# Optimization experiments

Hardware: AMD Instinct MI355X
Metric: run time of the kernel (lower is better)

The kernel has to match this reference:

```python
import jax, jax.numpy as jnp
import numpy as np

S, B, D, H, F = 2048, 2, 1024, 16, 4096
HD = D // H
EPS = 1e-5


def setup_inputs() -> dict:
    key = jax.random.key(0)
    ks = jax.random.split(key, 16)
    sc_d = 1.0 / np.sqrt(D)
    sc_f = 1.0 / np.sqrt(F)
    return {
        "src": jax.random.normal(ks[0], (S, B, D), jnp.float32),
        # attention projections: Linear weights stored as [in, out] (y = x @ W + b)
        "Wq": jax.random.normal(ks[1], (D, D), jnp.float32) * sc_d,
        "bq": jnp.zeros((D,), jnp.float32),
        "Wk": jax.random.normal(ks[2], (D, D), jnp.float32) * sc_d,
        "bk": jnp.zeros((D,), jnp.float32),
        "Wv": jax.random.normal(ks[3], (D, D), jnp.float32) * sc_d,
        "bv": jnp.zeros((D,), jnp.float32),
        "Wo": jax.random.normal(ks[4], (D, D), jnp.float32) * sc_d,
        "bo": jnp.zeros((D,), jnp.float32),
        # norm1
        "g1": jnp.ones((D,), jnp.float32),
        "be1": jnp.zeros((D,), jnp.float32),
        # FFN
        "W1": jax.random.normal(ks[5], (D, F), jnp.float32) * sc_d,
        "bf1": jnp.zeros((F,), jnp.float32),
        "W2": jax.random.normal(ks[6], (F, D), jnp.float32) * sc_f,
        "bf2": jnp.zeros((D,), jnp.float32),
        # norm2
        "g2": jnp.ones((D,), jnp.float32),
        "be2": jnp.zeros((D,), jnp.float32),
    }


def _layernorm(x, g, b):
    m = jnp.mean(x, axis=-1, keepdims=True)
    v = jnp.mean(jnp.square(x - m), axis=-1, keepdims=True)
    return (x - m) * jax.lax.rsqrt(v + EPS) * g + b


def reference(src, Wq, bq, Wk, bk, Wv, bv, Wo, bo, g1, be1, W1, bf1, W2, bf2, g2, be2):
    # --- self attention (dropout_p=0 / eval mode => dropouts are identity) ---
    scaling = float(HD) ** -0.5
    q = (src @ Wq + bq) * scaling            # [S,B,D]
    k = src @ Wk + bk
    v = src @ Wv + bv
    # split heads: torch view(S, B*H, hd) == reshape(S, B, H, hd)
    qh = q.reshape(S, B, H, HD)
    kh = k.reshape(S, B, H, HD)
    vh = v.reshape(S, B, H, HD)
    scores = jnp.einsum("sbhd,tbhd->bhst", qh, kh)      # [B,H,S,S]
    attn = jax.nn.softmax(scores, axis=-1)
    ctx = jnp.einsum("bhst,tbhd->sbhd", attn, vh).reshape(S, B, D)
    attn_out = ctx @ Wo + bo
    # residual + norm1
    x = _layernorm(src + attn_out, g1, be1)
    # FFN (ReLU)
    ff = jax.nn.relu(x @ W1 + bf1) @ W2 + bf2
    # residual + norm2
    return _layernorm(x + ff, g2, be2)
```

## Files before the change

### kernel.cpp

```cpp
#include <hip/hip_runtime.h>
#include <hip/hip_bf16.h>

#define S_  2048
#define B_  2
#define D_  1024
#define H_  16
#define F_  4096
#define HD_ 64
#define NT_ (S_*B_)

typedef __attribute__((ext_vector_type(8))) short short8;
typedef __attribute__((ext_vector_type(4))) short short4v;
typedef __attribute__((ext_vector_type(4))) float f32x4;

#define MFMA16x16x32(a,b,c) __builtin_amdgcn_mfma_f32_16x16x32_bf16((a),(b),(c),0,0,0)

#define AS1C(p) ((const __attribute__((address_space(1))) void*)(p))
#define AS3(p)  ((__attribute__((address_space(3))) void*)(p))

__device__ __forceinline__ short f2b(float f) {
  union { float f; unsigned u; } x; x.f = f;
  unsigned r = x.u + 0x7FFFu + ((x.u >> 16) & 1u);
  return (short)(r >> 16);
}
__device__ __forceinline__ float b2f(short u) {
  union { unsigned u; float f; } x; x.u = ((unsigned)(unsigned short)u) << 16;
  return x.f;
}
__device__ __forceinline__ unsigned cvtpk(float a, float b) {
  unsigned r;
  asm("v_cvt_pk_bf16_f32 %0, %1, %2" : "=v"(r) : "v"(a), "v"(b));
  return r;
}
__device__ __forceinline__ float exp2fast(float x) {
  float r;
  asm("v_exp_f32 %0, %1" : "=v"(r) : "v"(x));
  return r;
}

__global__ __launch_bounds__(256) void to_bf16_k(const float* __restrict__ in,
                                                 short* __restrict__ out) {
  int i = (blockIdx.x * 256 + threadIdx.x) * 8;
  float4 a = *(const float4*)(in + i);
  float4 b = *(const float4*)(in + i + 4);
  short8 o;
  o[0] = f2b(a.x); o[1] = f2b(a.y); o[2] = f2b(a.z); o[3] = f2b(a.w);
  o[4] = f2b(b.x); o[5] = f2b(b.y); o[6] = f2b(b.z); o[7] = f2b(b.w);
  *(short8*)(out + i) = o;
}

__global__ __launch_bounds__(256) void transpose_to_bf16(const float* __restrict__ W,
                                                         short* __restrict__ Wt,
                                                         int K, int N, int colbase, int outK) {
  __shared__ short t[32][33];
  int tx = threadIdx.x & 31, ty = threadIdx.x >> 5;
  int kbase = blockIdx.y * 32, nbase = blockIdx.x * 32;
#pragma unroll
  for (int yy = 0; yy < 4; ++yy) {
    int kk = ty + yy * 8;
    t[kk][tx] = f2b(W[(size_t)(kbase + kk) * N + nbase + tx]);
  }
  __syncthreads();
#pragma unroll
  for (int yy = 0; yy < 4; ++yy) {
    int nn = ty + yy * 8;
    Wt[(size_t)(nbase + nn + colbase) * outK + kbase + tx] = t[tx][nn];
  }
}

template<int MODE>
__global__ __launch_bounds__(256, 2) void gemm_bt(
    const short* __restrict__ A, const short* __restrict__ Bt,
    int M, int N, int K, int lda,
    const float* __restrict__ bias0, const float* __restrict__ bias1,
    const float* __restrict__ bias2,
    float* __restrict__ outf,
    short* __restrict__ outq, short* __restrict__ outk, short* __restrict__ outv) {
  __shared__ __align__(16) short As[128 * 64];
  __shared__ __align__(16) short Bs[128 * 64];
  int tid = threadIdx.x;
  int lane = tid & 63, w = tid >> 6;
  int g = lane >> 4, r = lane & 15;
  int wm = w >> 1, wn = w & 1;

  int gx = gridDim.x, gy = gridDim.y;
  int nwg = gx * gy * gridDim.z;
  int flat = (blockIdx.z * gy + blockIdx.y) * gx + blockIdx.x;
  int cpx = nwg >> 3;
  int swz = (flat & 7) * cpx + (flat >> 3);
  int z = swz / (gx * gy);
  int rem = swz - z * gx * gy;
  int row0 = (rem / gx) * 128;
  int col0 = (rem % gx) * 128;
  size_t koff = (size_t)z * K;

  f32x4 acc[4][4];
#pragma unroll
  for (int m = 0; m < 4; ++m)
#pragma unroll
    for (int n = 0; n < 4; ++n) acc[m][n] = (f32x4){0.f, 0.f, 0.f, 0.f};

  for (int kt = 0; kt < K; kt += 64) {
#pragma unroll
    for (int p = 0; p < 4; ++p) {
      int idx = tid + p * 256;
      int row = idx >> 3, c = idx & 7;
      int scol = ((c ^ (row & 7)) << 3);
      __builtin_amdgcn_global_load_lds(AS1C(A  + (size_t)(row0 + row) * lda + koff + kt + scol),
                                       AS3(As + idx * 8), 16, 0, 0);
      __builtin_amdgcn_global_load_lds(AS1C(Bt + (size_t)(col0 + row) * lda + koff + kt + scol),
                                       AS3(Bs + idx * 8), 16, 0, 0);
    }
    __syncthreads();
    short8 af[4][2], bfr[4][2];
#pragma unroll
    for (int m = 0; m < 4; ++m)
#pragma unroll
      for (int kk = 0; kk < 2; ++kk) {
        int row = wm * 64 + m * 16 + r;
        af[m][kk] = *(const short8*)(As + row * 64 + (((kk * 4 + g) ^ (r & 7)) << 3));
      }
#pragma unroll
    for (int n = 0; n < 4; ++n)
#pragma unroll
      for (int kk = 0; kk < 2; ++kk) {
        int row = wn * 64 + n * 16 + r;
        bfr[n][kk] = *(const short8*)(Bs + row * 64 + (((kk * 4 + g) ^ (r & 7)) << 3));
      }
#pragma unroll
    for (int m = 0; m < 4; ++m)
#pragma unroll
      for (int n = 0; n < 4; ++n)
#pragma unroll
        for (int kk = 0; kk < 2; ++kk)
          acc[m][n] = MFMA16x16x32(af[m][kk], bfr[n][kk], acc[m][n]);
    __syncthreads();
  }

  int rb = row0 + wm * 64, cb = col0 + wn * 64;
#pragma unroll
  for (int m = 0; m < 4; ++m) {
#pragma unroll
    for (int n = 0; n < 4; ++n) {
#pragma unroll
      for (int j = 0; j < 4; ++j) {
        int row = rb + m * 16 + g * 4 + j;
        int col = cb + n * 16 + r;
        float v = acc[m][n][j];
        if (MODE == 0) {
          int s = row >> 1, b = row & 1;
          if (col < 1024) {
            float q = (v + bias0[col]) * (0.125f * 1.44269504088896f);
            int h = col >> 6, hd = col & 63;
            outq[((size_t)(b * H_ + h) * S_ + s) * HD_ + hd] = f2b(q);
          } else if (col < 2048) {
            int c2 = col - 1024;
            float kk = v + bias1[c2];
            int h = c2 >> 6, hd = c2 & 63;
            outk[((size_t)(b * H_ + h) * S_ + s) * HD_ + hd] = f2b(kk);
          } else {
            int c2 = col - 2048;
            float vv = v + bias2[c2];
            int h = c2 >> 6, hd = c2 & 63;
            outv[((size_t)(b * H_ + h) * HD_ + hd) * S_ + s] = f2b(vv);
          }
        } else if (MODE == 2) {
          size_t o = (size_t)row * N + col;
          float t = v + bias0[col];
          outq[o] = f2b(t > 0.f ? t : 0.f);
        } else {
          outf[(size_t)z * M * N + (size_t)row * N + col] = v;
        }
      }
    }
  }
}

__global__ __launch_bounds__(256, 4) void flash_attn(const short* __restrict__ Q,
                                                     const short* __restrict__ Kb,
                                                     const short* __restrict__ Vt,
                                                     short* __restrict__ ctx) {
  __shared__ __align__(16) short Ks[2][64 * 64];
  __shared__ __align__(16) short Vs[2][64 * 64];
  __shared__ __align__(16) short P[4][16][64];
  int tid = threadIdx.x;
  int lane = tid & 63, w = tid >> 6;
  int g = lane >> 4, r = lane & 15;
  int f = blockIdx.x;
  int xcd = f & 7, loc = f >> 3;
  int bh = xcd * 4 + (loc >> 5);
  int qt = loc & 31;
  const short* qp = Q  + (size_t)bh * S_ * HD_;
  const short* kp = Kb + (size_t)bh * S_ * HD_;
  const short* vp = Vt + (size_t)bh * HD_ * S_;
  int q0 = qt * 64 + w * 16;

  short8 qf[2];
#pragma unroll
  for (int kk = 0; kk < 2; ++kk)
    qf[kk] = *(const short8*)(qp + (size_t)(q0 + r) * HD_ + kk * 32 + g * 8);

  f32x4 acc[4];
  float mi = -1e30f, li = 0.f;
#pragma unroll
  for (int db = 0; db < 4; ++db) acc[db] = (f32x4){0.f, 0.f, 0.f, 0.f};

#pragma unroll
  for (int p = 0; p < 2; ++p) {
    int idx = tid + p * 256;
    int row = idx >> 3, c = idx & 7;
    int scol = ((c ^ (row & 7)) << 3);
    __builtin_amdgcn_global_load_lds(AS1C(kp + (size_t)row * HD_ + scol),
                                     AS3(&Ks[0][0] + idx * 8), 16, 0, 0);
    __builtin_amdgcn_global_load_lds(AS1C(vp + (size_t)row * S_ + scol),
                                     AS3(&Vs[0][0] + idx * 8), 16, 0, 0);
  }
  __syncthreads();

  int cur = 0;
  for (int t = 0; t < S_ / 64; ++t) {
    if (t + 1 < S_ / 64) {
      int kv1 = (t + 1) * 64;
#pragma unroll
      for (int p = 0; p < 2; ++p) {
        int idx = tid + p * 256;
        int row = idx >> 3, c = idx & 7;
        int scol = ((c ^ (row & 7)) << 3);
        __builtin_amdgcn_global_load_lds(AS1C(kp + (size_t)(kv1 + row) * HD_ + scol),
                                         AS3(&Ks[cur ^ 1][0] + idx * 8), 16, 0, 0);
        __builtin_amdgcn_global_load_lds(AS1C(vp + (size_t)row * S_ + kv1 + scol),
                                         AS3(&Vs[cur ^ 1][0] + idx * 8), 16, 0, 0);
      }
    }
    const short* Kc = &Ks[cur][0];
    const short* Vc = &Vs[cur][0];
    short8 kf[4][2];
#pragma unroll
    for (int kb = 0; kb < 4; ++kb)
#pragma unroll
      for (int kk = 0; kk < 2; ++kk) {
        int row = kb * 16 + r;
        kf[kb][kk] = *(const short8*)(Kc + row * 64 + (((kk * 4 + g) ^ (r & 7)) << 3));
      }

    f32x4 st[4];
    __builtin_amdgcn_s_setprio(1);
#pragma unroll
    for (int kb = 0; kb < 4; ++kb) {
      f32x4 tt = (f32x4){0.f, 0.f, 0.f, 0.f};
      tt = MFMA16x16x32(kf[kb][0], qf[0], tt);
      tt = MFMA16x16x32(kf[kb][1], qf[1], tt);
      st[kb] = tt;
    }
    __builtin_amdgcn_s_setprio(0);

    float pm = st[0][0];
#pragma unroll
    for (int kb = 0; kb < 4; ++kb)
#pragma unroll
      for (int j = 0; j < 4; ++j) pm = fmaxf(pm, st[kb][j]);
    if (!__all(pm <= mi + 8.0f)) {
      pm = fmaxf(pm, __shfl_xor(pm, 16));
      pm = fmaxf(pm, __shfl_xor(pm, 32));
      float mn = fmaxf(mi, pm);
      float sc = exp2fast(mi - mn);
      mi = mn;
      li *= sc;
#pragma unroll
      for (int db = 0; db < 4; ++db)
#pragma unroll
        for (int j = 0; j < 4; ++j) acc[db][j] *= sc;
    }
    float rs = 0.f;
#pragma unroll
    for (int kb = 0; kb < 4; ++kb)
#pragma unroll
      for (int j = 0; j < 4; ++j) {
        float p0 = exp2fast(st[kb][j] - mi);
        st[kb][j] = p0;
        rs += p0;
      }
    li += rs;

#pragma unroll
    for (int kb = 0; kb < 4; ++kb) {
      unsigned w0 = cvtpk(st[kb][0], st[kb][1]);
      unsigned w1 = cvtpk(st[kb][2], st[kb][3]);
      unsigned long long pw = (unsigned long long)w0 | ((unsigned long long)w1 << 32);
      int col = (kb * 16 + g * 4) ^ ((r & 7) << 3);
      *(unsigned long long*)(&P[w][r][0] + col) = pw;
    }

    short8 vf[4][2];
#pragma unroll
    for (int db = 0; db < 4; ++db)
#pragma unroll
      for (int ks = 0; ks < 2; ++ks) {
        int row = db * 16 + r;
        vf[db][ks] = *(const short8*)(Vc + row * 64 + (((ks * 4 + g) ^ (r & 7)) << 3));
      }
    short8 pf[2];
#pragma unroll
    for (int ks = 0; ks < 2; ++ks) {
      int col = (ks * 32 + g * 8) ^ ((r & 7) << 3);
      pf[ks] = *(const short8*)(&P[w][r][0] + col);
    }

    __builtin_amdgcn_s_setprio(1);
#pragma unroll
    for (int db = 0; db < 4; ++db) {
      acc[db] = MFMA16x16x32(vf[db][0], pf[0], acc[db]);
      acc[db] = MFMA16x16x32(vf[db][1], pf[1], acc[db]);
    }
    __builtin_amdgcn_s_setprio(0);

    __syncthreads();
    cur ^= 1;
  }

  li += __shfl_xor(li, 16);
  li += __shfl_xor(li, 32);

  int b = bh >> 4, h = bh & 15;
  float inv = 1.0f / li;
  int s = q0 + r;
  int token = s * B_ + b;
#pragma unroll
  for (int db = 0; db < 4; ++db) {
    unsigned w0 = cvtpk(acc[db][0] * inv, acc[db][1] * inv);
    unsigned w1 = cvtpk(acc[db][2] * inv, acc[db][3] * inv);
    unsigned long long pw = (unsigned long long)w0 | ((unsigned long long)w1 << 32);
    *(unsigned long long*)(ctx + (size_t)token * D_ + h * 64 + db * 16 + g * 4) = pw;
  }
}

template<int RESBF16, int WF, int WB>
__global__ __launch_bounds__(256) void layernorm_fused(
    const float* __restrict__ p0, const float* __restrict__ p1,
    const float* __restrict__ bias,
    const float* __restrict__ residf, const short* __restrict__ residb,
    const float* __restrict__ gm, const float* __restrict__ bt,
    float* __restrict__ of, short* __restrict__ ob) {
  __shared__ float r1[4], r2[4];
  int row = blockIdx.x, tid = threadIdx.x;
  size_t base = (size_t)row * D_ + tid * 4;
  float4 a = *(const float4*)(p0 + base);
  float4 b = *(const float4*)(p1 + base);
  float4 bi = *(const float4*)(bias + tid * 4);
  float4 v;
  if (RESBF16) {
    short4v rb = *(const short4v*)(residb + base);
    v.x = a.x + b.x + bi.x + b2f(rb[0]);
    v.y = a.y + b.y + bi.y + b2f(rb[1]);
    v.z = a.z + b.z + bi.z + b2f(rb[2]);
    v.w = a.w + b.w + bi.w + b2f(rb[3]);
  } else {
    float4 rf = *(const float4*)(residf + base);
    v.x = a.x + b.x + bi.x + rf.x;
    v.y = a.y + b.y + bi.y + rf.y;
    v.z = a.z + b.z + bi.z + rf.z;
    v.w = a.w + b.w + bi.w + rf.w;
  }
  float s1 = v.x + v.y + v.z + v.w;
  float s2 = v.x * v.x + v.y * v.y + v.z * v.z + v.w * v.w;
#pragma unroll
  for (int off = 32; off > 0; off >>= 1) {
    s1 += __shfl_xor(s1, off, 64);
    s2 += __shfl_xor(s2, off, 64);
  }
  int wid = tid >> 6;
  if ((tid & 63) == 0) { r1[wid] = s1; r2[wid] = s2; }
  __syncthreads();
  s1 = r1[0] + r1[1] + r1[2] + r1[3];
  s2 = r2[0] + r2[1] + r2[2] + r2[3];
  float mean = s1 * (1.0f / D_);
  float var = s2 * (1.0f / D_) - mean * mean;
  float rstd = rsqrtf(var + 1e-5f);
  float4 gv = *(const float4*)(gm + tid * 4);
  float4 bv = *(const float4*)(bt + tid * 4);
  float o0 = (v.x - mean) * rstd * gv.x + bv.x;
  float o1 = (v.y - mean) * rstd * gv.y + bv.y;
  float o2 = (v.z - mean) * rstd * gv.z + bv.z;
  float o3 = (v.w - mean) * rstd * gv.w + bv.w;
  if (WF) *(float4*)(of + base) = make_float4(o0, o1, o2, o3);
  if (WB) {
    short4v o;
    o[0] = f2b(o0); o[1] = f2b(o1); o[2] = f2b(o2); o[3] = f2b(o3);
    *(short4v*)(ob + base) = o;
  }
}

extern "C" void kernel_launch(void* const* d_in, const int* in_sizes, int n_in,
                              void* d_out, int out_size, void* d_ws, size_t ws_size,
                              hipStream_t stream) {
  const float* src = (const float*)d_in[0];
  const float* Wq  = (const float*)d_in[1];
  const float* bq  = (const float*)d_in[2];
  const float* Wk  = (const float*)d_in[3];
  const float* bk  = (const float*)d_in[4];
  const float* Wv  = (const float*)d_in[5];
  const float* bv  = (const float*)d_in[6];
  const float* Wo  = (const float*)d_in[7];
  const float* bo  = (const float*)d_in[8];
  const float* g1  = (const float*)d_in[9];
  const float* be1 = (const float*)d_in[10];
  const float* W1  = (const float*)d_in[11];
  const float* bf1 = (const float*)d_in[12];
  const float* W2  = (const float*)d_in[13];
  const float* bf2 = (const float*)d_in[14];
  const float* g2  = (const float*)d_in[15];
  const float* be2 = (const float*)d_in[16];
  float* out = (float*)d_out;
  char* ws = (char*)d_ws;

  const size_t MiB = 1024 * 1024;
  short* Wqkv_t = (short*)(ws + 0 * MiB);
  short* Wo_t   = (short*)(ws + 6 * MiB);
  short* W1_t   = (short*)(ws + 8 * MiB);
  short* W2_t   = (short*)(ws + 16 * MiB);
  short* xb     = (short*)(ws + 24 * MiB);
  short* x1b    = (short*)(ws + 24 * MiB);
  short* ctx    = (short*)(ws + 32 * MiB);
  short* qb_    = (short*)(ws + 40 * MiB);
  short* kb_    = (short*)(ws + 48 * MiB);
  short* vb_    = (short*)(ws + 56 * MiB);
  short* hid    = (short*)(ws + 32 * MiB);
  float* part   = (float*)(ws + 64 * MiB);
  float* part1  = part + (size_t)NT_ * D_;

  to_bf16_k<<<2048, 256, 0, stream>>>(src, xb);

  transpose_to_bf16<<<dim3(32, 32),  256, 0, stream>>>(Wq, Wqkv_t, 1024, 1024, 0,    1024);
  transpose_to_bf16<<<dim3(32, 32),  256, 0, stream>>>(Wk, Wqkv_t, 1024, 1024, 1024, 1024);
  transpose_to_bf16<<<dim3(32, 32),  256, 0, stream>>>(Wv, Wqkv_t, 1024, 1024, 2048, 1024);
  transpose_to_bf16<<<dim3(32, 32),  256, 0, stream>>>(Wo, Wo_t,   1024, 1024, 0,    1024);
  transpose_to_bf16<<<dim3(128, 32), 256, 0, stream>>>(W1, W1_t,   1024, 4096, 0,    1024);
  transpose_to_bf16<<<dim3(32, 128), 256, 0, stream>>>(W2, W2_t,   4096, 1024, 0,    4096);

  gemm_bt<0><<<dim3(24, 32, 1), 256, 0, stream>>>(xb, Wqkv_t, NT_, 3072, 1024, 1024,
                                                  bq, bk, bv, nullptr, qb_, kb_, vb_);
  flash_attn<<<1024, 256, 0, stream>>>(qb_, kb_, vb_, ctx);
  gemm_bt<3><<<dim3(8, 32, 2), 256, 0, stream>>>(ctx, Wo_t, NT_, 1024, 512, 1024,
                                                 nullptr, nullptr, nullptr, part,
                                                 nullptr, nullptr, nullptr);
  layernorm_fused<0, 0, 1><<<NT_, 256, 0, stream>>>(part, part1, bo, src, nullptr,
                                                    g1, be1, nullptr, x1b);
  gemm_bt<2><<<dim3(32, 32, 1), 256, 0, stream>>>(x1b, W1_t, NT_, 4096, 1024, 1024,
                                                  bf1, nullptr, nullptr, nullptr,
                                                  hid, nullptr, nullptr);
  gemm_bt<3><<<dim3(8, 32, 2), 256, 0, stream>>>(hid, W2_t, NT_, 1024, 2048, 4096,
                                                 nullptr, nullptr, nullptr, part,
                                                 nullptr, nullptr, nullptr);
  layernorm_fused<1, 1, 0><<<NT_, 256, 0, stream>>>(part, part1, bf2, nullptr, x1b,
                                                    g2, be2, out, nullptr);
}
```

Measured before the change: 237.2 us.

## Enlarge flash attention query tile to 128 rows with 8 waves per block

Flash attention blocks now hold 8 waves (512 threads) covering 128 query rows instead of 64, halving grid size to 512. Each K/V tile staged into LDS is now shared by twice as many query rows, halving global K/V traffic and load instructions per thread. The trade-off is fewer blocks (512 over 256 CUs), which risks tail imbalance and lower occupancy flexibility, and a bigger P buffer in LDS.

After: 239.0 us. Within noise of the previous version (+0.8%).

```diff
diff --git a/kernel.cpp b/kernel.cpp
--- a/kernel.cpp
+++ b/kernel.cpp
@@ -176,24 +176,24 @@
   }
 }
 
-__global__ __launch_bounds__(256, 4) void flash_attn(const short* __restrict__ Q,
+__global__ __launch_bounds__(512, 6) void flash_attn(const short* __restrict__ Q,
                                                      const short* __restrict__ Kb,
                                                      const short* __restrict__ Vt,
                                                      short* __restrict__ ctx) {
   __shared__ __align__(16) short Ks[2][64 * 64];
   __shared__ __align__(16) short Vs[2][64 * 64];
-  __shared__ __align__(16) short P[4][16][64];
+  __shared__ __align__(16) short P[8][16][64];
   int tid = threadIdx.x;
   int lane = tid & 63, w = tid >> 6;
   int g = lane >> 4, r = lane & 15;
   int f = blockIdx.x;
   int xcd = f & 7, loc = f >> 3;
-  int bh = xcd * 4 + (loc >> 5);
-  int qt = loc & 31;
+  int bh = xcd * 4 + (loc >> 4);
+  int qt = loc & 15;
   const short* qp = Q  + (size_t)bh * S_ * HD_;
   const short* kp = Kb + (size_t)bh * S_ * HD_;
   const short* vp = Vt + (size_t)bh * HD_ * S_;
-  int q0 = qt * 64 + w * 16;
+  int q0 = qt * 128 + w * 16;
 
   short8 qf[2];
 #pragma unroll
@@ -205,32 +205,23 @@
 #pragma unroll
   for (int db = 0; db < 4; ++db) acc[db] = (f32x4){0.f, 0.f, 0.f, 0.f};
 
-#pragma unroll
-  for (int p = 0; p < 2; ++p) {
-    int idx = tid + p * 256;
-    int row = idx >> 3, c = idx & 7;
-    int scol = ((c ^ (row & 7)) << 3);
-    __builtin_amdgcn_global_load_lds(AS1C(kp + (size_t)row * HD_ + scol),
-                                     AS3(&Ks[0][0] + idx * 8), 16, 0, 0);
-    __builtin_amdgcn_global_load_lds(AS1C(vp + (size_t)row * S_ + scol),
-                                     AS3(&Vs[0][0] + idx * 8), 16, 0, 0);
-  }
+  int srow = tid >> 3, sc = tid & 7;
+  int scol = ((sc ^ (srow & 7)) << 3);
+
+  __builtin_amdgcn_global_load_lds(AS1C(kp + (size_t)srow * HD_ + scol),
+                                   AS3(&Ks[0][0] + tid * 8), 16, 0, 0);
+  __builtin_amdgcn_global_load_lds(AS1C(vp + (size_t)srow * S_ + scol),
+                                   AS3(&Vs[0][0] + tid * 8), 16, 0, 0);
   __syncthreads();
 
   int cur = 0;
   for (int t = 0; t < S_ / 64; ++t) {
     if (t + 1 < S_ / 64) {
       int kv1 = (t + 1) * 64;
-#pragma unroll
-      for (int p = 0; p < 2; ++p) {
-        int idx = tid + p * 256;
-        int row = idx >> 3, c = idx & 7;
-        int scol = ((c ^ (row & 7)) << 3);
-        __builtin_amdgcn_global_load_lds(AS1C(kp + (size_t)(kv1 + row) * HD_ + scol),
-                                         AS3(&Ks[cur ^ 1][0] + idx * 8), 16, 0, 0);
-        __builtin_amdgcn_global_load_lds(AS1C(vp + (size_t)row * S_ + kv1 + scol),
-                                         AS3(&Vs[cur ^ 1][0] + idx * 8), 16, 0, 0);
-      }
+      __builtin_amdgcn_global_load_lds(AS1C(kp + (size_t)(kv1 + srow) * HD_ + scol),
+                                       AS3(&Ks[cur ^ 1][0] + tid * 8), 16, 0, 0);
+      __builtin_amdgcn_global_load_lds(AS1C(vp + (size_t)srow * S_ + kv1 + scol),
+                                       AS3(&Vs[cur ^ 1][0] + tid * 8), 16, 0, 0);
     }
     const short* Kc = &Ks[cur][0];
     const short* Vc = &Vs[cur][0];
@@ -263,13 +254,13 @@
       pm = fmaxf(pm, __shfl_xor(pm, 16));
       pm = fmaxf(pm, __shfl_xor(pm, 32));
       float mn = fmaxf(mi, pm);
-      float sc = exp2fast(mi - mn);
+      float sc2 = exp2fast(mi - mn);
       mi = mn;
-      li *= sc;
+      li *= sc2;
 #pragma unroll
       for (int db = 0; db < 4; ++db)
 #pragma unroll
-        for (int j = 0; j < 4; ++j) acc[db][j] *= sc;
+        for (int j = 0; j < 4; ++j) acc[db][j] *= sc2;
     }
     float rs = 0.f;
 #pragma unroll
@@ -439,7 +430,7 @@
 
   gemm_bt<0><<<dim3(24, 32, 1), 256, 0, stream>>>(xb, Wqkv_t, NT_, 3072, 1024, 1024,
                                                   bq, bk, bv, nullptr, qb_, kb_, vb_);
-  flash_attn<<<1024, 256, 0, stream>>>(qb_, kb_, vb_, ctx);
+  flash_attn<<<512, 512, 0, stream>>>(qb_, kb_, vb_, ctx);
   gemm_bt<3><<<dim3(8, 32, 2), 256, 0, stream>>>(ctx, Wo_t, NT_, 1024, 512, 1024,
                                                  nullptr, nullptr, nullptr, part,
                                                  nullptr, nullptr, nullptr);
```
